# Kernel optimization log

Measured on AMD Instinct MI355X. Metric: run time of the kernel, lower is better.

The kernel has to match this reference:

```python
import jax, jax.numpy as jnp
import numpy as np
from jax import lax

K, N = 256, 65536

def setup_inputs() -> dict:
    key = jax.random.key(0)
    k1, k2, k3 = jax.random.split(key, 3)
    # obs: non-negative event counts [K, N]
    obs = jax.random.uniform(k1, (K, N), dtype=jnp.float32) * 4.0
    # Beta ~ U(1, 3) [K]
    Beta = 1.0 + 2.0 * jax.random.uniform(k2, (K,), dtype=jnp.float32)
    # Alpha ~ U(0, 0.01) [K, K]
    Alpha = 0.01 * jax.random.uniform(k3, (K, K), dtype=jnp.float32)
    return {"obs": obs, "Beta": Beta, "Alpha": Alpha}

def reference(obs, Beta, Alpha):
    # obs: [K, N], Beta: [K], Alpha: [K, K]
    Kk, Nn = obs.shape
    Mu0 = obs.mean(axis=1) / 10.0 + 0.01            # [K] background rate
    decay = jnp.exp(-Beta)                          # [K]

    # Exponential kernel sum S[t] = sum_{tp<t} obs[:,tp] * Beta * exp(-(t-tp)*Beta)
    # admits recursion H[t] = exp(-Beta) * (H[t-1] + obs[:, t-1]), S[t] = Beta * H[t]
    def step(h, o_prev):
        h_new = decay * (h + o_prev)
        return h_new, h_new

    _, H = lax.scan(step, jnp.zeros((Kk,), obs.dtype), obs[:, :Nn - 1].T)  # [N-1, K]
    S = H * Beta                                    # [N-1, K]
    # lam1[:, t] = softplus(Alpha @ S[t]) for t >= 1; lam1[:, 0] = 0 (by original code)
    lam = jax.nn.softplus(jnp.einsum('jk,tk->tj', Alpha, S))  # [N-1, K]
    lams1 = jnp.concatenate([jnp.zeros((Kk, 1), obs.dtype), lam.T], axis=1)  # [K, N]
    lams0 = jnp.broadcast_to(Mu0[:, None], (Kk, Nn))          # [K, N]

    Nloglams = obs * jnp.log(lams0 + lams1 + 1e-5)
    loglik = (Nloglams - lams0 - lams1).sum()
    return loglik, lams0, lams1
```

## Files before the change

kernel.cpp:

```cpp
#include <hip/hip_runtime.h>
#include <math.h>

#define KK 256
#define NN 65536
#define TT 64
#define WW 16
#define TPAD 264

typedef __bf16 bf16x8 __attribute__((ext_vector_type(8)));
typedef float f32x4 __attribute__((ext_vector_type(4)));

__global__ __launch_bounds__(256) void prep_kernel(const float* __restrict__ obs,
                                                   const float* __restrict__ Alpha,
                                                   float* __restrict__ mu0,
                                                   __bf16* __restrict__ AlphaB) {
  const int j = blockIdx.x;
  const int tid = threadIdx.x;
  AlphaB[(size_t)j * KK + tid] = (__bf16)Alpha[(size_t)j * KK + tid];
  const float4* p = (const float4*)(obs + (size_t)j * NN) + tid;
  float s = 0.f;
#pragma unroll
  for (int i = 0; i < 64; ++i) {
    float4 v = p[i * 256];
    s += (v.x + v.y) + (v.z + v.w);
  }
  __shared__ float red[256];
  red[tid] = s;
  __syncthreads();
  for (int off = 128; off > 0; off >>= 1) {
    if (tid < off) red[tid] += red[tid + off];
    __syncthreads();
  }
  if (tid == 0) mu0[j] = red[0] * (1.0f / NN) * 0.1f + 0.01f;
}

__global__ __launch_bounds__(256, 2) void main_kernel(const float* __restrict__ obs,
                                                      const float* __restrict__ Beta,
                                                      const float* __restrict__ mu0,
                                                      const __bf16* __restrict__ AlphaB,
                                                      float* __restrict__ out,
                                                      float* __restrict__ bpart) {
  __shared__ __bf16 Slds[TT][TPAD];
  const int tid = threadIdx.x;
  const int bid = blockIdx.x;
  const int tb = ((bid & 7) << 7) | (bid >> 3);
  const int t0 = tb * TT;

  {
    const int k = tid;
    const float beta = Beta[k];
    const float decay = expf(-beta);
    const float* row = obs + (size_t)k * NN;
    float g = 0.f;
    if (t0 > 0) {
      const float4* p = (const float4*)(row + t0 - WW);
#pragma unroll
      for (int i = 0; i < WW / 4; ++i) {
        float4 v = p[i];
        g = decay * (g + v.x);
        g = decay * (g + v.y);
        g = decay * (g + v.z);
        g = decay * (g + v.w);
      }
    }
    Slds[0][k] = (__bf16)(beta * g);
    const float4* q = (const float4*)(row + t0);
#pragma unroll
    for (int i = 0; i < 15; ++i) {
      float4 v = q[i];
      g = decay * (g + v.x); Slds[4 * i + 1][k] = (__bf16)(beta * g);
      g = decay * (g + v.y); Slds[4 * i + 2][k] = (__bf16)(beta * g);
      g = decay * (g + v.z); Slds[4 * i + 3][k] = (__bf16)(beta * g);
      g = decay * (g + v.w); Slds[4 * i + 4][k] = (__bf16)(beta * g);
    }
    {
      float4 v = q[15];
      g = decay * (g + v.x); Slds[61][k] = (__bf16)(beta * g);
      g = decay * (g + v.y); Slds[62][k] = (__bf16)(beta * g);
      g = decay * (g + v.z); Slds[63][k] = (__bf16)(beta * g);
    }
  }
  __syncthreads();

  const int wave = tid >> 6;
  const int lane = tid & 63;
  const int lquad = lane >> 4;
  const int l16 = lane & 15;

  f32x4 acc[4][4];
#pragma unroll
  for (int a = 0; a < 4; ++a)
#pragma unroll
    for (int b = 0; b < 4; ++b) acc[a][b] = (f32x4){0.f, 0.f, 0.f, 0.f};

  const __bf16* Abase = AlphaB + (size_t)(wave * 64 + l16) * KK + lquad * 8;
  for (int k0 = 0; k0 < KK; k0 += 32) {
    bf16x8 afrag[4], bfrag[4];
#pragma unroll
    for (int js = 0; js < 4; ++js)
      afrag[js] = *(const bf16x8*)(Abase + (size_t)js * 16 * KK + k0);
#pragma unroll
    for (int ts = 0; ts < 4; ++ts)
      bfrag[ts] = *(const bf16x8*)&Slds[ts * 16 + l16][k0 + lquad * 8];
#pragma unroll
    for (int js = 0; js < 4; ++js)
#pragma unroll
      for (int ts = 0; ts < 4; ++ts)
        acc[js][ts] = __builtin_amdgcn_mfma_f32_16x16x32_bf16(
            afrag[js], bfrag[ts], acc[js][ts], 0, 0, 0);
  }

  float partial = 0.f;
  float* lams0 = out + 1;
  float* lams1 = out + 1 + (size_t)KK * NN;
#pragma unroll
  for (int js = 0; js < 4; ++js) {
#pragma unroll
    for (int r = 0; r < 4; ++r) {
      const int j = wave * 64 + js * 16 + lquad * 4 + r;
      const float m = mu0[j];
      const size_t rowoff = (size_t)j * NN + t0 + l16;
#pragma unroll
      for (int ts = 0; ts < 4; ++ts) {
        float v = acc[js][ts][r];
        float lam = v + __logf(1.f + __expf(-v));
        if (t0 + ts * 16 + l16 == 0) lam = 0.f;
        lams1[rowoff + ts * 16] = lam;
        lams0[rowoff + ts * 16] = m;
        const float o = obs[rowoff + ts * 16];
        partial += o * __logf(m + lam + 1e-5f) - m - lam;
      }
    }
  }

#pragma unroll
  for (int off = 32; off > 0; off >>= 1)
    partial += __shfl_down(partial, off, 64);
  __syncthreads();
  float* red = (float*)&Slds[0][0];
  if (lane == 0) red[wave] = partial;
  __syncthreads();
  if (tid == 0) bpart[bid] = (red[0] + red[1]) + (red[2] + red[3]);
}

__global__ __launch_bounds__(256) void finish_kernel(const float* __restrict__ bpart,
                                                     float* __restrict__ out) {
  const int tid = threadIdx.x;
  f32x4 v = ((const f32x4*)bpart)[tid];
  float s = (v[0] + v[1]) + (v[2] + v[3]);
#pragma unroll
  for (int off = 32; off > 0; off >>= 1)
    s += __shfl_down(s, off, 64);
  __shared__ float red[4];
  if ((tid & 63) == 0) red[tid >> 6] = s;
  __syncthreads();
  if (tid == 0) out[0] = (red[0] + red[1]) + (red[2] + red[3]);
}

extern "C" void kernel_launch(void* const* d_in, const int* in_sizes, int n_in,
                              void* d_out, int out_size, void* d_ws, size_t ws_size,
                              hipStream_t stream) {
  const float* obs   = (const float*)d_in[0];
  const float* Beta  = (const float*)d_in[1];
  const float* Alpha = (const float*)d_in[2];
  float* out = (float*)d_out;

  float* mu0 = (float*)d_ws;
  __bf16* AlphaB = (__bf16*)(mu0 + 256);
  float* bpart = (float*)(AlphaB + (size_t)KK * KK);

  hipLaunchKernelGGL(prep_kernel, dim3(KK), dim3(256), 0, stream, obs, Alpha,
                     mu0, AlphaB);
  hipLaunchKernelGGL(main_kernel, dim3(NN / TT), dim3(256), 0, stream,
                     obs, Beta, mu0, AlphaB, out, bpart);
  hipLaunchKernelGGL(finish_kernel, dim3(1), dim3(256), 0, stream, bpart, out);
}
```

Baseline: 243.7 us.

## Move lams0 broadcast fill into prep kernel and double time tile per block

Writing the constant lams0 rows moves out of the main kernel's scattered epilogue and into the prep kernel, which already holds mu0 and fills each row with contiguous float4 stores. The main kernel now uses 512-thread blocks covering 128 timesteps, with two waves sharing each Alpha row group, so half as many blocks are launched and Alpha fragment loads are amortised. The prep kernel grows to 512 threads to cover the extra writes. The cost is doubled LDS per block, which may reduce occupancy, and a prep kernel that now does much more work with only 256 blocks.

```diff
diff --git a/kernel.cpp b/kernel.cpp
--- a/kernel.cpp
+++ b/kernel.cpp
@@ -3,38 +3,47 @@
 
 #define KK 256
 #define NN 65536
-#define TT 64
+#define TT 128
 #define WW 16
 #define TPAD 264
 
 typedef __bf16 bf16x8 __attribute__((ext_vector_type(8)));
 typedef float f32x4 __attribute__((ext_vector_type(4)));
 
-__global__ __launch_bounds__(256) void prep_kernel(const float* __restrict__ obs,
+__global__ __launch_bounds__(512) void prep_kernel(const float* __restrict__ obs,
                                                    const float* __restrict__ Alpha,
                                                    float* __restrict__ mu0,
-                                                   __bf16* __restrict__ AlphaB) {
+                                                   __bf16* __restrict__ AlphaB,
+                                                   float* __restrict__ out) {
   const int j = blockIdx.x;
   const int tid = threadIdx.x;
-  AlphaB[(size_t)j * KK + tid] = (__bf16)Alpha[(size_t)j * KK + tid];
+  if (tid < KK) AlphaB[(size_t)j * KK + tid] = (__bf16)Alpha[(size_t)j * KK + tid];
   const float4* p = (const float4*)(obs + (size_t)j * NN) + tid;
   float s = 0.f;
 #pragma unroll
-  for (int i = 0; i < 64; ++i) {
-    float4 v = p[i * 256];
+  for (int i = 0; i < 32; ++i) {
+    float4 v = p[i * 512];
     s += (v.x + v.y) + (v.z + v.w);
   }
-  __shared__ float red[256];
+  __shared__ float red[512];
   red[tid] = s;
   __syncthreads();
-  for (int off = 128; off > 0; off >>= 1) {
+  for (int off = 256; off > 0; off >>= 1) {
     if (tid < off) red[tid] += red[tid + off];
     __syncthreads();
   }
-  if (tid == 0) mu0[j] = red[0] * (1.0f / NN) * 0.1f + 0.01f;
+  const float m = red[0] * (1.0f / NN) * 0.1f + 0.01f;
+  if (tid == 0) mu0[j] = m;
+
+  float* row0 = out + 1 + (size_t)j * NN;
+  if (tid < 3) row0[tid] = m;
+  if (tid == 3) row0[NN - 1] = m;
+  float4* p4 = (float4*)(row0 + 3);
+  const float4 mv = {m, m, m, m};
+  for (int i = tid; i < (NN - 4) / 4; i += 512) p4[i] = mv;
 }
 
-__global__ __launch_bounds__(256, 2) void main_kernel(const float* __restrict__ obs,
+__global__ __launch_bounds__(512, 4) void main_kernel(const float* __restrict__ obs,
                                                       const float* __restrict__ Beta,
                                                       const float* __restrict__ mu0,
                                                       const __bf16* __restrict__ AlphaB,
@@ -43,17 +52,19 @@
   __shared__ __bf16 Slds[TT][TPAD];
   const int tid = threadIdx.x;
   const int bid = blockIdx.x;
-  const int tb = ((bid & 7) << 7) | (bid >> 3);
+  const int tb = ((bid & 7) << 6) | (bid >> 3);
   const int t0 = tb * TT;
 
   {
-    const int k = tid;
+    const int k = tid & 255;
+    const int c = tid >> 8;
+    const int tbase = t0 + 64 * c;
     const float beta = Beta[k];
     const float decay = expf(-beta);
     const float* row = obs + (size_t)k * NN;
     float g = 0.f;
-    if (t0 > 0) {
-      const float4* p = (const float4*)(row + t0 - WW);
+    if (tbase > 0) {
+      const float4* p = (const float4*)(row + tbase - WW);
 #pragma unroll
       for (int i = 0; i < WW / 4; ++i) {
         float4 v = p[i];
@@ -63,26 +74,28 @@
         g = decay * (g + v.w);
       }
     }
-    Slds[0][k] = (__bf16)(beta * g);
-    const float4* q = (const float4*)(row + t0);
+    const int r0 = 64 * c;
+    Slds[r0][k] = (__bf16)(beta * g);
+    const float4* q = (const float4*)(row + tbase);
 #pragma unroll
     for (int i = 0; i < 15; ++i) {
       float4 v = q[i];
-      g = decay * (g + v.x); Slds[4 * i + 1][k] = (__bf16)(beta * g);
-      g = decay * (g + v.y); Slds[4 * i + 2][k] = (__bf16)(beta * g);
-      g = decay * (g + v.z); Slds[4 * i + 3][k] = (__bf16)(beta * g);
-      g = decay * (g + v.w); Slds[4 * i + 4][k] = (__bf16)(beta * g);
+      g = decay * (g + v.x); Slds[r0 + 4 * i + 1][k] = (__bf16)(beta * g);
+      g = decay * (g + v.y); Slds[r0 + 4 * i + 2][k] = (__bf16)(beta * g);
+      g = decay * (g + v.z); Slds[r0 + 4 * i + 3][k] = (__bf16)(beta * g);
+      g = decay * (g + v.w); Slds[r0 + 4 * i + 4][k] = (__bf16)(beta * g);
     }
     {
       float4 v = q[15];
-      g = decay * (g + v.x); Slds[61][k] = (__bf16)(beta * g);
-      g = decay * (g + v.y); Slds[62][k] = (__bf16)(beta * g);
-      g = decay * (g + v.z); Slds[63][k] = (__bf16)(beta * g);
+      g = decay * (g + v.x); Slds[r0 + 61][k] = (__bf16)(beta * g);
+      g = decay * (g + v.y); Slds[r0 + 62][k] = (__bf16)(beta * g);
+      g = decay * (g + v.z); Slds[r0 + 63][k] = (__bf16)(beta * g);
     }
   }
   __syncthreads();
 
   const int wave = tid >> 6;
+  const int wj = wave & 3, wc = wave >> 2;
   const int lane = tid & 63;
   const int lquad = lane >> 4;
   const int l16 = lane & 15;
@@ -93,7 +106,7 @@
 #pragma unroll
     for (int b = 0; b < 4; ++b) acc[a][b] = (f32x4){0.f, 0.f, 0.f, 0.f};
 
-  const __bf16* Abase = AlphaB + (size_t)(wave * 64 + l16) * KK + lquad * 8;
+  const __bf16* Abase = AlphaB + (size_t)(wj * 64 + l16) * KK + lquad * 8;
   for (int k0 = 0; k0 < KK; k0 += 32) {
     bf16x8 afrag[4], bfrag[4];
 #pragma unroll
@@ -101,7 +114,7 @@
       afrag[js] = *(const bf16x8*)(Abase + (size_t)js * 16 * KK + k0);
 #pragma unroll
     for (int ts = 0; ts < 4; ++ts)
-      bfrag[ts] = *(const bf16x8*)&Slds[ts * 16 + l16][k0 + lquad * 8];
+      bfrag[ts] = *(const bf16x8*)&Slds[wc * 64 + ts * 16 + l16][k0 + lquad * 8];
 #pragma unroll
     for (int js = 0; js < 4; ++js)
 #pragma unroll
@@ -111,22 +124,21 @@
   }
 
   float partial = 0.f;
-  float* lams0 = out + 1;
   float* lams1 = out + 1 + (size_t)KK * NN;
+  const int tcol = t0 + wc * 64;
 #pragma unroll
   for (int js = 0; js < 4; ++js) {
 #pragma unroll
     for (int r = 0; r < 4; ++r) {
-      const int j = wave * 64 + js * 16 + lquad * 4 + r;
+      const int j = wj * 64 + js * 16 + lquad * 4 + r;
       const float m = mu0[j];
-      const size_t rowoff = (size_t)j * NN + t0 + l16;
+      const size_t rowoff = (size_t)j * NN + tcol + l16;
 #pragma unroll
       for (int ts = 0; ts < 4; ++ts) {
         float v = acc[js][ts][r];
         float lam = v + __logf(1.f + __expf(-v));
-        if (t0 + ts * 16 + l16 == 0) lam = 0.f;
+        if (tcol + ts * 16 + l16 == 0) lam = 0.f;
         lams1[rowoff + ts * 16] = lam;
-        lams0[rowoff + ts * 16] = m;
         const float o = obs[rowoff + ts * 16];
         partial += o * __logf(m + lam + 1e-5f) - m - lam;
       }
@@ -140,14 +152,18 @@
   float* red = (float*)&Slds[0][0];
   if (lane == 0) red[wave] = partial;
   __syncthreads();
-  if (tid == 0) bpart[bid] = (red[0] + red[1]) + (red[2] + red[3]);
+  if (tid == 0) {
+    float s = 0.f;
+#pragma unroll
+    for (int w = 0; w < 8; ++w) s += red[w];
+    bpart[bid] = s;
+  }
 }
 
 __global__ __launch_bounds__(256) void finish_kernel(const float* __restrict__ bpart,
                                                      float* __restrict__ out) {
   const int tid = threadIdx.x;
-  f32x4 v = ((const f32x4*)bpart)[tid];
-  float s = (v[0] + v[1]) + (v[2] + v[3]);
+  float s = bpart[tid] + bpart[tid + 256];
 #pragma unroll
   for (int off = 32; off > 0; off >>= 1)
     s += __shfl_down(s, off, 64);
@@ -169,9 +185,9 @@
   __bf16* AlphaB = (__bf16*)(mu0 + 256);
   float* bpart = (float*)(AlphaB + (size_t)KK * KK);
 
-  hipLaunchKernelGGL(prep_kernel, dim3(KK), dim3(256), 0, stream, obs, Alpha,
-                     mu0, AlphaB);
-  hipLaunchKernelGGL(main_kernel, dim3(NN / TT), dim3(256), 0, stream,
+  hipLaunchKernelGGL(prep_kernel, dim3(KK), dim3(512), 0, stream, obs, Alpha,
+                     mu0, AlphaB, out);
+  hipLaunchKernelGGL(main_kernel, dim3(NN / TT), dim3(512), 0, stream,
                      obs, Beta, mu0, AlphaB, out, bpart);
   hipLaunchKernelGGL(finish_kernel, dim3(1), dim3(256), 0, stream, bpart, out);
 }
```

Measured after the change: 231.1 us. -5.2%, faster.
